# Performance work log

Measured on AMD Instinct MI355X. Metric: run time of the kernel, lower is better.

The kernel has to match this reference:

```python
import jax, jax.numpy as jnp
import numpy as np

C, NSET, K, GC = 64, 32, 3, 4
G = C // GC          # 16 KBA groups
EPS = 1e-6


def conv2d(x, w, b=None, groups=1, padding=0):
    out = jax.lax.conv_general_dilated(
        x, w, (1, 1), [(padding, padding), (padding, padding)],
        dimension_numbers=('NCHW', 'OIHW', 'NCHW'), feature_group_count=groups)
    if b is not None:
        out = out + b[None, :, None, None]
    return out


def layernorm2d(x, w, b):
    mu = jnp.mean(x, axis=1, keepdims=True)
    var = jnp.var(x, axis=1, keepdims=True)
    return (x - mu) / jnp.sqrt(var + EPS) * w[None, :, None, None] + b[None, :, None, None]


def simple_gate(x):
    a, b = jnp.split(x, 2, axis=1)
    return a * b


def kba(x, att, kb_b, kb_w):
    # x: [B,C,H,W], att: [B,nset,H,W], kb_b: [1,nset,C], kb_w: [1,nset,C*(C//G)*K*K]
    B, C_, H, W = x.shape
    KK = K * K
    cg = C_ // G  # channels per group
    att2 = att.reshape(B, NSET, H * W).transpose(0, 2, 1)            # [B,HW,nset]
    bias = att2 @ kb_b[0]                                             # [B,HW,C]
    attk = (att2 @ kb_w[0]).reshape(B, H * W, G, cg, cg * KK)         # per-pixel kernels
    pad = K // 2
    xp = jnp.pad(x, ((0, 0), (0, 0), (pad, pad), (pad, pad)))
    # torch.unfold ordering: feature index = c*KK + ki*K + kj
    patches = jnp.stack([xp[:, :, i:i + H, j:j + W]
                         for i in range(K) for j in range(K)], axis=2)  # [B,C,KK,H,W]
    uf = patches.reshape(B, G, cg * KK, H * W).transpose(0, 3, 1, 2)    # [B,HW,G,cg*KK]
    out = jnp.einsum('bpgod,bpgd->bpgo', attk, uf).reshape(B, H * W, C_) + bias
    return out.transpose(0, 2, 1).reshape(B, C_, H, W)


def fca(x, fc1_w, fc1_b, fc2_w, fc2_b, fsca_w, fsca_b):
    f = jnp.fft.fft2(x, norm='ortho')                      # over (H,W)
    cf = jnp.concatenate([f.real, f.imag], axis=1)         # [B,2C,H,W]
    t = conv2d(simple_gate(conv2d(cf, fc1_w, fc1_b)), fc2_w, fc2_b)
    r, im = jnp.split(t, 2, axis=1)
    ra = conv2d(jnp.mean(r, axis=(2, 3), keepdims=True), fsca_w, fsca_b)
    ia = conv2d(jnp.mean(im, axis=(2, 3), keepdims=True), fsca_w, fsca_b)
    fn = (r + r * ra) + 1j * (im + im * ia)
    return jnp.abs(jnp.fft.ifft2(fn, norm='ortho'))


def reference(inp, n1_w, n1_b, n2_w, n2_b, sca_w, sca_b, c11a_w, c11a_b, c11b_w, c11b_b,
              c1_w, c1_b, c21_w, c21_b, c2a_w, c2a_b, c2c_w, c2c_b, c211_w, c211_b,
              c3_w, c3_b, kb_w, kb_b, ga1, attgamma, beta, gamma,
              fc1_w, fc1_b, fc2_w, fc2_b, fsca_w, fsca_b):
    x = layernorm2d(inp, n1_w, n1_b)
    sca = conv2d(jnp.mean(x, axis=(2, 3), keepdims=True), sca_w, sca_b)
    x1 = conv2d(conv2d(x, c11a_w, c11a_b), c11b_w, c11b_b, groups=C // 4, padding=2)
    att = conv2d(simple_gate(conv2d(x, c2a_w, c2a_b, groups=32, padding=1)),
                 c2c_w, c2c_b) * attgamma + conv2d(x, c211_w, c211_b)
    uf = conv2d(conv2d(x, c1_w, c1_b), c21_w, c21_b, groups=C, padding=1)
    xk = kba(uf, att, kb_b, kb_w) * ga1 + uf
    x = xk * x1 * sca
    x = conv2d(x, c3_w, c3_b)
    y = inp + x * beta
    z = fca(layernorm2d(y, n2_w, n2_b), fc1_w, fc1_b, fc2_w, fc2_b, fsca_w, fsca_b)
    return y + z * gamma


def setup_inputs() -> dict:
    key = jax.random.key(0)
    B, H, W = 2, 160, 160
    ks = jax.random.split(key, 32)
    def rn(i, shape, s=0.05):
        return jax.random.normal(ks[i], shape, dtype=jnp.float32) * s
    return dict(
        inp=rn(0, (B, C, H, W), 1.0),
        n1_w=jnp.ones((C,), jnp.float32), n1_b=jnp.zeros((C,), jnp.float32),
        n2_w=jnp.ones((C,), jnp.float32), n2_b=jnp.zeros((C,), jnp.float32),
        sca_w=rn(1, (C, C, 1, 1)), sca_b=rn(2, (C,)),
        c11a_w=rn(3, (C, C, 1, 1)), c11a_b=rn(4, (C,)),
        c11b_w=rn(5, (C, 4, 5, 5)), c11b_b=rn(6, (C,)),
        c1_w=rn(7, (C, C, 1, 1)), c1_b=rn(8, (C,)),
        c21_w=rn(9, (C, 1, 3, 3)), c21_b=rn(10, (C,)),
        c2a_w=rn(11, (32, 2, 3, 3)), c2a_b=rn(12, (32,)),
        c2c_w=rn(13, (NSET, 16, 1, 1)), c2c_b=rn(14, (NSET,)),
        c211_w=rn(15, (NSET, C, 1, 1)), c211_b=rn(16, (NSET,)),
        c3_w=rn(17, (C, C, 1, 1)), c3_b=rn(18, (C,)),
        kb_w=rn(19, (1, NSET, C * (C // G) * K * K)),
        kb_b=rn(20, (1, NSET, C)),
        ga1=jnp.full((1, C, 1, 1), 0.01, jnp.float32),
        attgamma=jnp.full((1, NSET, 1, 1), 0.01, jnp.float32),
        beta=jnp.full((1, C, 1, 1), 0.01, jnp.float32),
        gamma=jnp.full((1, C, 1, 1), 0.01, jnp.float32),
        fc1_w=rn(21, (4 * C, 2 * C, 1, 1)), fc1_b=rn(22, (4 * C,)),
        fc2_w=rn(23, (2 * C, 2 * C, 1, 1)), fc2_b=rn(24, (2 * C,)),
        fsca_w=rn(25, (C, C, 1, 1)), fsca_b=rn(26, (C,)),
    )
```

## Files before the change

kernel.cpp:

```cpp
#include <hip/hip_runtime.h>
#include <hip/hip_bf16.h>

typedef __hip_bfloat16 bf16;
typedef __attribute__((ext_vector_type(8))) short short8;
typedef __attribute__((ext_vector_type(4))) float f32x4;
typedef __attribute__((ext_vector_type(4))) unsigned short u16x4;

#define Hh 160
#define Wd 160
#define HWp (Hh*Wd)
#define Bn 2
#define Cc 64
#define NPIX (Bn*HWp)
#define SCL 0.07905694150420949f
#define TWO_PI_160 0.039269908169872414f

static __device__ __forceinline__ float b2f(bf16 x) { return __bfloat162float(x); }
static __device__ __forceinline__ bf16 f2b(float f) { return __float2bfloat16(f); }
static __device__ __forceinline__ unsigned short f2bu(float f) {
  union { bf16 h; unsigned short u; } z; z.h = __float2bfloat16(f); return z.u;
}
static __device__ __forceinline__ float ubf(unsigned short u) {
  union { unsigned int i; float f; } z; z.i = ((unsigned int)u) << 16; return z.f;
}

__global__ void k_ln(const float* __restrict__ in, const float* __restrict__ w,
                     const float* __restrict__ bb, bf16* __restrict__ out) {
  __shared__ float2 sm[4][64];
  int t = threadIdx.x;
  int pxl = t & 63, cq = t >> 6;
  int pix = blockIdx.x * 64 + pxl;
  int b = pix / HWp, p = pix - b * HWp;
  const float* src = in + ((size_t)b * Cc + cq * 16) * HWp + p;
  float v[16];
  float s = 0.f, s2 = 0.f;
  #pragma unroll
  for (int i = 0; i < 16; i++) {
    v[i] = src[(size_t)i * HWp];
    s += v[i]; s2 += v[i] * v[i];
  }
  sm[cq][pxl] = make_float2(s, s2);
  __syncthreads();
  float S = 0.f, S2 = 0.f;
  #pragma unroll
  for (int k = 0; k < 4; k++) { float2 z = sm[k][pxl]; S += z.x; S2 += z.y; }
  float mu = S * (1.f / 64.f);
  float var = S2 * (1.f / 64.f) - mu * mu;
  float rs = rsqrtf(fmaxf(var, 0.f) + 1e-6f);
  bf16* dst = out + ((size_t)b * Cc + cq * 16) * HWp + p;
  #pragma unroll
  for (int i = 0; i < 16; i++) {
    int c = cq * 16 + i;
    dst[(size_t)i * HWp] = f2b((v[i] - mu) * rs * w[c] + bb[c]);
  }
}

__global__ void k_meanhw(const bf16* __restrict__ in, float* __restrict__ out) {
  int bc = blockIdx.x;
  const bf16* src = in + (size_t)bc * HWp;
  int t = threadIdx.x;
  float s = 0.f;
  for (int i = t; i < HWp; i += 256) s += b2f(src[i]);
  __shared__ float sm[256];
  sm[t] = s; __syncthreads();
  for (int off = 128; off; off >>= 1) { if (t < off) sm[t] += sm[t + off]; __syncthreads(); }
  if (t == 0) out[bc] = sm[0] * (1.f / HWp);
}

__global__ void k_meanhw2(const bf16* __restrict__ in0, const bf16* __restrict__ in1,
                          float* __restrict__ out) {
  int bc = blockIdx.x;
  const bf16* src = (bc < 128) ? (in0 + (size_t)bc * HWp) : (in1 + (size_t)(bc - 128) * HWp);
  int t = threadIdx.x;
  float s = 0.f;
  for (int i = t; i < HWp; i += 256) s += b2f(src[i]);
  __shared__ float sm[256];
  sm[t] = s; __syncthreads();
  for (int off = 128; off; off >>= 1) { if (t < off) sm[t] += sm[t + off]; __syncthreads(); }
  if (t == 0) out[bc] = sm[0] * (1.f / HWp);
}

__global__ void k_small_mv(const float* __restrict__ xin, const float* __restrict__ w,
                           const float* __restrict__ bias, float* __restrict__ out, int addone) {
  int t = threadIdx.x;
  int b = t >> 6, o = t & 63;
  float acc = bias[o];
  for (int k = 0; k < 64; k++) acc += w[o * 64 + k] * xin[b * 64 + k];
  out[t] = addone ? (1.f + acc) : acc;
}

__global__ void k_small_mv2(const float* __restrict__ xin, const float* __restrict__ w,
                            const float* __restrict__ bias, float* __restrict__ out) {
  int t = threadIdx.x;
  int half = t >> 7, r = t & 127;
  int b = r >> 6, o = r & 63;
  const float* x = xin + half * 128 + b * 64;
  float acc = bias[o];
  for (int k = 0; k < 64; k++) acc += w[o * 64 + k] * x[k];
  out[half * 128 + r] = 1.f + acc;
}

__global__ void k_c2a4(const bf16* __restrict__ in, const float* __restrict__ w,
                       const float* __restrict__ bias, bf16* __restrict__ out) {
  int t = threadIdx.x;
  int o = blockIdx.y, b = blockIdx.z;
  int pq = blockIdx.x * 256 + t;
  int h = pq / 40, x4 = (pq - h * 40) * 4;
  float bs = bias[o];
  float acc[4] = {bs, bs, bs, bs};
  #pragma unroll
  for (int ci = 0; ci < 2; ci++) {
    const unsigned short* src = (const unsigned short*)in + ((size_t)b * Cc + o * 2 + ci) * HWp;
    float wv[9];
    #pragma unroll
    for (int i = 0; i < 9; i++) wv[i] = w[(o * 2 + ci) * 9 + i];
    #pragma unroll
    for (int ki = 0; ki < 3; ki++) {
      int hh = h + ki - 1;
      if ((unsigned)hh >= Hh) continue;
      const unsigned short* row = src + hh * Wd + x4;
      float v[6];
      u16x4 m = *(const u16x4*)row;
      v[1] = ubf(m[0]); v[2] = ubf(m[1]); v[3] = ubf(m[2]); v[4] = ubf(m[3]);
      v[0] = (x4 > 0) ? ubf(row[-1]) : 0.f;
      v[5] = (x4 + 4 < Wd) ? ubf(row[4]) : 0.f;
      #pragma unroll
      for (int j = 0; j < 4; j++)
        #pragma unroll
        for (int kj = 0; kj < 3; kj++)
          acc[j] = fmaf(wv[ki * 3 + kj], v[j + kj], acc[j]);
    }
  }
  u16x4 pk;
  #pragma unroll
  for (int j = 0; j < 4; j++) pk[j] = f2bu(acc[j]);
  *(u16x4*)((unsigned short*)out + ((size_t)b * 32 + o) * HWp + h * Wd + x4) = pk;
}

__global__ void k_c21dw4(const bf16* __restrict__ in, const float* __restrict__ w,
                         const float* __restrict__ bias, bf16* __restrict__ out) {
  int t = threadIdx.x;
  int c = blockIdx.y, b = blockIdx.z;
  int pq = blockIdx.x * 256 + t;
  int h = pq / 40, x4 = (pq - h * 40) * 4;
  const unsigned short* src = (const unsigned short*)in + ((size_t)b * Cc + c) * HWp;
  float wv[9];
  #pragma unroll
  for (int i = 0; i < 9; i++) wv[i] = w[c * 9 + i];
  float bs = bias[c];
  float acc[4] = {bs, bs, bs, bs};
  #pragma unroll
  for (int ki = 0; ki < 3; ki++) {
    int hh = h + ki - 1;
    if ((unsigned)hh >= Hh) continue;
    const unsigned short* row = src + hh * Wd + x4;
    float v[6];
    u16x4 m = *(const u16x4*)row;
    v[1] = ubf(m[0]); v[2] = ubf(m[1]); v[3] = ubf(m[2]); v[4] = ubf(m[3]);
    v[0] = (x4 > 0) ? ubf(row[-1]) : 0.f;
    v[5] = (x4 + 4 < Wd) ? ubf(row[4]) : 0.f;
    #pragma unroll
    for (int j = 0; j < 4; j++)
      #pragma unroll
      for (int kj = 0; kj < 3; kj++)
        acc[j] = fmaf(wv[ki * 3 + kj], v[j + kj], acc[j]);
  }
  u16x4 pk;
  #pragma unroll
  for (int j = 0; j < 4; j++) pk[j] = f2bu(acc[j]);
  *(u16x4*)((unsigned short*)out + ((size_t)b * Cc + c) * HWp + h * Wd + x4) = pk;
}

__global__ void k_prep_all(const float* __restrict__ kbw, const float* __restrict__ kbb,
                           short* __restrict__ kbwF,
                           const float* __restrict__ fc1w, const float* __restrict__ fc2w,
                           short* __restrict__ wAf1, short* __restrict__ wAf2,
                           short* __restrict__ cosF, short* __restrict__ sinF,
                           const float* __restrict__ c11aw, const float* __restrict__ c1w,
                           const float* __restrict__ c3w, const float* __restrict__ c2cw,
                           const float* __restrict__ c211w, const float* __restrict__ attg,
                           short* __restrict__ wA_c11a, short* __restrict__ wA_c1,
                           short* __restrict__ wA_c3, short* __restrict__ wA_att) {
  int i = blockIdx.x * 256 + threadIdx.x;
  if (i < 81920) {
    int g = i / 5120, r = i - g * 5120;
    float v = 0.f;
    if (r < 4096) {
      int j = r & 7, lane = (r >> 3) & 63, mt = r >> 9;
      int m = mt * 16 + (lane & 15);
      int s = m >> 2, o = m & 3;
      int k = (lane >> 4) * 8 + j;
      v = kbw[s * 2304 + g * 144 + o * 36 + k];
    } else {
      int r2 = r - 4096;
      int j = r2 & 7, n = (r2 >> 3) & 15, mt = r2 >> 7;
      int m = mt * 16 + n;
      int s = m >> 2, o = m & 3;
      int k = 32 + j;
      if (k < 36) v = kbw[s * 2304 + g * 144 + o * 36 + k];
      else if (k == 36) v = kbb[s * 64 + g * 4 + o];
    }
    kbwF[i] = (short)f2bu(v);
  } else if (i < 131072) {
    int i1 = i - 81920;
    if (i1 < 32768) {
      int j = i1 & 7, lane = (i1 >> 3) & 63, fk = i1 >> 9;
      int kc = fk & 3, mt = fk >> 2;
      int o = mt * 16 + (lane & 15);
      int k = kc * 32 + (lane >> 4) * 8 + j;
      wAf1[i1] = (short)f2bu(fc1w[o * 128 + k]);
    } else {
      int i2 = i1 - 32768;
      int j = i2 & 7, lane = (i2 >> 3) & 63, fk = i2 >> 9;
      int kc = fk & 3, mt = fk >> 2;
      int o = mt * 16 + (lane & 15);
      int k = kc * 32 + (lane >> 4) * 8 + j;
      wAf2[i2] = (short)f2bu(fc2w[o * 128 + k]);
    }
  } else if (i < 156672) {
    int i2 = i - 131072;
    int j = i2 & 7, lane = (i2 >> 3) & 63, fk = i2 >> 9;
    int kc = fk % 5, ct = fk / 5;
    int c = ct * 16 + (lane & 15);
    int bb2 = kc * 32 + (lane >> 4) * 8 + j;
    int m = (bb2 * c) % 160;
    float sv, cv;
    __sincosf((float)m * TWO_PI_160, &sv, &cv);
    cosF[i2] = (short)f2bu(cv);
    sinF[i2] = (short)f2bu(sv);
  } else {
    int i3 = i - 156672;
    if (i3 < 12288) {
      int wi = i3 / 4096, r = i3 - wi * 4096;
      int j = r & 7, lane = (r >> 3) & 63, fk = r >> 9;
      int kc = fk & 1, mt = fk >> 1;
      int o = mt * 16 + (lane & 15);
      int k = kc * 32 + (lane >> 4) * 8 + j;
      const float* w = (wi == 0) ? c11aw : (wi == 1) ? c1w : c3w;
      short* dst = (wi == 0) ? wA_c11a : (wi == 1) ? wA_c1 : wA_c3;
      dst[r] = (short)f2bu(w[o * 64 + k]);
    } else {
      int r = i3 - 12288;
      int j = r & 7, lane = (r >> 3) & 63, fk = r >> 9;
      int kc = fk % 3, mt = fk / 3;
      int s = mt * 16 + (lane & 15);
      int k = kc * 32 + (lane >> 4) * 8 + j;
      float v;
      if (k < 16) v = c2cw[s * 16 + k] * attg[s];
      else if (k < 32) v = 0.f;
      else v = c211w[s * 64 + (k - 32)];
      wA_att[r] = (short)f2bu(v);
    }
  }
}

__global__ __launch_bounds__(256) void k_conv1x1_mfma(
    const bf16* __restrict__ in, const short* __restrict__ wA,
    const float* __restrict__ bias, bf16* __restrict__ out) {
  int b = blockIdx.z;
  int lane = threadIdx.x & 63, w = threadIdx.x >> 6;
  int px = blockIdx.x * 64 + w * 16 + (lane & 15);
  int q = lane >> 4;
  const unsigned short* src = (const unsigned short*)in + (size_t)b * Cc * HWp;
  const short8* wf = (const short8*)wA;
  f32x4 acc[4];
  #pragma unroll
  for (int mt = 0; mt < 4; mt++) acc[mt] = (f32x4){0.f, 0.f, 0.f, 0.f};
  #pragma unroll
  for (int kc = 0; kc < 2; kc++) {
    short8 bfv;
    #pragma unroll
    for (int j = 0; j < 8; j++) bfv[j] = (short)src[(size_t)(kc * 32 + q * 8 + j) * HWp + px];
    #pragma unroll
    for (int mt = 0; mt < 4; mt++) {
      short8 af = wf[(mt * 2 + kc) * 64 + lane];
      acc[mt] = __builtin_amdgcn_mfma_f32_16x16x32_bf16(af, bfv, acc[mt], 0, 0, 0);
    }
  }
  unsigned short* dst = (unsigned short*)out + (size_t)b * Cc * HWp;
  #pragma unroll
  for (int mt = 0; mt < 4; mt++)
    #pragma unroll
    for (int j = 0; j < 4; j++) {
      int o = mt * 16 + q * 4 + j;
      dst[(size_t)o * HWp + px] = f2bu(acc[mt][j] + bias[o]);
    }
}

__global__ __launch_bounds__(256) void k_c3y_mfma(
    const bf16* __restrict__ in, const short* __restrict__ wA,
    const float* __restrict__ bias, const float* __restrict__ beta,
    const float* __restrict__ inp, float* __restrict__ y) {
  int b = blockIdx.z;
  int lane = threadIdx.x & 63, w = threadIdx.x >> 6;
  int px = blockIdx.x * 64 + w * 16 + (lane & 15);
  int q = lane >> 4;
  const unsigned short* src = (const unsigned short*)in + (size_t)b * Cc * HWp;
  const short8* wf = (const short8*)wA;
  f32x4 acc[4];
  #pragma unroll
  for (int mt = 0; mt < 4; mt++) acc[mt] = (f32x4){0.f, 0.f, 0.f, 0.f};
  #pragma unroll
  for (int kc = 0; kc < 2; kc++) {
    short8 bfv;
    #pragma unroll
    for (int j = 0; j < 8; j++) bfv[j] = (short)src[(size_t)(kc * 32 + q * 8 + j) * HWp + px];
    #pragma unroll
    for (int mt = 0; mt < 4; mt++) {
      short8 af = wf[(mt * 2 + kc) * 64 + lane];
      acc[mt] = __builtin_amdgcn_mfma_f32_16x16x32_bf16(af, bfv, acc[mt], 0, 0, 0);
    }
  }
  #pragma unroll
  for (int mt = 0; mt < 4; mt++)
    #pragma unroll
    for (int j = 0; j < 4; j++) {
      int o = mt * 16 + q * 4 + j;
      size_t oi = ((size_t)b * Cc + o) * HWp + px;
      y[oi] = inp[oi] + (acc[mt][j] + bias[o]) * beta[o];
    }
}

__global__ __launch_bounds__(256) void k_att_mfma(
    const bf16* __restrict__ g, const bf16* __restrict__ x,
    const short* __restrict__ wA, const float* __restrict__ c2cb,
    const float* __restrict__ c211b, const float* __restrict__ attg,
    bf16* __restrict__ att) {
  int b = blockIdx.z;
  int lane = threadIdx.x & 63, w = threadIdx.x >> 6;
  int px = blockIdx.x * 64 + w * 16 + (lane & 15);
  int q = lane >> 4;
  const unsigned short* gs = (const unsigned short*)g + (size_t)b * 32 * HWp;
  const unsigned short* xs = (const unsigned short*)x + (size_t)b * Cc * HWp;
  const short8* wf = (const short8*)wA;
  f32x4 acc[2];
  acc[0] = (f32x4){0.f, 0.f, 0.f, 0.f};
  acc[1] = (f32x4){0.f, 0.f, 0.f, 0.f};
  {
    short8 bfv;
    #pragma unroll
    for (int j = 0; j < 8; j++) {
      int k = q * 8 + j;
      short v = 0;
      if (q < 2) {
        float gv = ubf(gs[(size_t)k * HWp + px]) * ubf(gs[(size_t)(16 + k) * HWp + px]);
        v = (short)f2bu(gv);
      }
      bfv[j] = v;
    }
    #pragma unroll
    for (int mt = 0; mt < 2; mt++) {
      short8 af = wf[(mt * 3 + 0) * 64 + lane];
      acc[mt] = __builtin_amdgcn_mfma_f32_16x16x32_bf16(af, bfv, acc[mt], 0, 0, 0);
    }
  }
  #pragma unroll
  for (int kc = 1; kc < 3; kc++) {
    short8 bfv;
    #pragma unroll
    for (int j = 0; j < 8; j++)
      bfv[j] = (short)xs[(size_t)((kc - 1) * 32 + q * 8 + j) * HWp + px];
    #pragma unroll
    for (int mt = 0; mt < 2; mt++) {
      short8 af = wf[(mt * 3 + kc) * 64 + lane];
      acc[mt] = __builtin_amdgcn_mfma_f32_16x16x32_bf16(af, bfv, acc[mt], 0, 0, 0);
    }
  }
  unsigned short* dst = (unsigned short*)att + (size_t)b * 32 * HWp;
  #pragma unroll
  for (int mt = 0; mt < 2; mt++)
    #pragma unroll
    for (int j = 0; j < 4; j++) {
      int s = mt * 16 + q * 4 + j;
      dst[(size_t)s * HWp + px] = f2bu(acc[mt][j] + c2cb[s] * attg[s] + c211b[s]);
    }
}

__global__ __launch_bounds__(256) void k_c11b_direct(
    const bf16* __restrict__ t1, const float* __restrict__ w,
    const float* __restrict__ bias, bf16* __restrict__ out) {
  __shared__ float xs[4 * 20 * 68];
  __shared__ float wsm[4 * 5 * 4 * 5];
  __shared__ float bsm[4];
  int bz = blockIdx.z;
  int b = bz >> 4, g = bz & 15;
  int h0 = blockIdx.y * 16;
  int w0 = blockIdx.x * 64;
  int t = threadIdx.x;
  for (int i = t; i < 400; i += 256) {
    int kj = i % 5, rem = i / 5;
    int o = rem & 3; rem >>= 2;
    int ki = rem % 5, ci = rem / 5;
    wsm[i] = w[((g * 4 + o) * 4 + ci) * 25 + ki * 5 + kj];
  }
  if (t < 4) bsm[t] = bias[g * 4 + t];
  const unsigned short* src = (const unsigned short*)t1 + ((size_t)b * Cc + g * 4) * HWp;
  for (int i = t; i < 4 * 20 * 68; i += 256) {
    int ci = i / 1360, rem2 = i - ci * 1360;
    int r = rem2 / 68, col = rem2 - r * 68;
    int hh = h0 + r - 2, ww = w0 + col - 2;
    float v = 0.f;
    if ((unsigned)hh < Hh && (unsigned)ww < Wd)
      v = ubf(src[(size_t)ci * HWp + hh * Wd + ww]);
    xs[i] = v;
  }
  __syncthreads();
  int wq = t & 15, hq = t >> 4;
  float acc[4][4];
  #pragma unroll
  for (int o = 0; o < 4; o++)
    #pragma unroll
    for (int j = 0; j < 4; j++) acc[o][j] = bsm[o];
  #pragma unroll
  for (int ci = 0; ci < 4; ci++) {
    #pragma unroll
    for (int ki = 0; ki < 5; ki++) {
      const float* wrow = &wsm[(ci * 5 + ki) * 20];
      float wv[20];
      #pragma unroll
      for (int x = 0; x < 20; x++) wv[x] = wrow[x];
      const float* xrow = &xs[ci * 1360 + (hq + ki) * 68 + wq * 4];
      float xv[8];
      #pragma unroll
      for (int x = 0; x < 8; x++) xv[x] = xrow[x];
      #pragma unroll
      for (int o = 0; o < 4; o++)
        #pragma unroll
        for (int j = 0; j < 4; j++)
          #pragma unroll
          for (int kj = 0; kj < 5; kj++)
            acc[o][j] = fmaf(wv[o * 5 + kj], xv[j + kj], acc[o][j]);
    }
  }
  int width = Wd - w0;
  if (wq * 4 < width) {
    unsigned short* dst = (unsigned short*)out + ((size_t)b * Cc + g * 4) * HWp
                        + (h0 + hq) * Wd + w0 + wq * 4;
    #pragma unroll
    for (int o = 0; o < 4; o++) {
      u16x4 pk;
      #pragma unroll
      for (int j = 0; j < 4; j++) pk[j] = f2bu(acc[o][j]);
      *(u16x4*)(dst + (size_t)o * HWp) = pk;
    }
  }
}

__global__ __launch_bounds__(256) void k_kba_mfma(
    const bf16* __restrict__ uf, const bf16* __restrict__ att,
    const bf16* __restrict__ x1, const float* __restrict__ scaV,
    const short* __restrict__ kbwF, const float* __restrict__ ga1,
    bf16* __restrict__ out) {
  __shared__ short8 fragL[1280];
  __shared__ unsigned short patchL[8 * 3 * 66];
  __shared__ unsigned short attL[64][33];
  int bz = blockIdx.z;
  int b = bz >> 3, gp = bz & 7;
  int h = blockIdx.y;
  int w0 = blockIdx.x * 64;
  int width = min(64, Wd - w0);
  int t = threadIdx.x;
  int c0 = gp * 8;
  const short8* src8 = (const short8*)kbwF + (size_t)gp * 1280;
  #pragma unroll
  for (int i = 0; i < 5; i++) fragL[t + i * 256] = src8[t + i * 256];
  const unsigned short* uf_u = (const unsigned short*)uf;
  for (int i = t; i < 8 * 3 * 66; i += 256) {
    int cl = i / 198, rem = i - cl * 198;
    int r = rem / 66, col = rem - r * 66;
    int hh = h + r - 1, ww = w0 + col - 1;
    unsigned short v = 0;
    if ((unsigned)hh < Hh && (unsigned)ww < Wd)
      v = uf_u[((size_t)b * Cc + c0 + cl) * HWp + hh * Wd + ww];
    patchL[i] = v;
  }
  const unsigned short* att_u = (const unsigned short*)att + (size_t)b * 32 * HWp;
  for (int i = t; i < 64 * 32; i += 256) {
    int px = i & 63, s = i >> 6;
    unsigned short v = 0;
    if (px < width) v = att_u[(size_t)s * HWp + h * Wd + w0 + px];
    attL[px][s] = v;
  }
  __syncthreads();
  int lane = t & 63, w = t >> 6;
  int n = lane & 15, q = lane >> 4;
  int pxl = w * 16 + n;
  float attR[8];
  #pragma unroll
  for (int mt = 0; mt < 8; mt++) attR[mt] = ubf(attL[pxl][4 * mt + q]);
  int offA[8];
  #pragma unroll
  for (int j = 0; j < 8; j++) {
    int k = q * 8 + j;
    int ci = k / 9, r = k - ci * 9, ki = r / 3, kj = r - ki * 3;
    offA[j] = ci * 198 + ki * 66 + pxl + kj;
  }
  int offB[4];
  #pragma unroll
  for (int j = 0; j < 4; j++) {
    int k = 32 + j, r = k - 27, ki = r / 3, kj = r - ki * 3;
    offB[j] = 3 * 198 + ki * 66 + pxl + kj;
  }
  const unsigned short* x1u = (const unsigned short*)x1 + (size_t)b * Cc * HWp + h * Wd + w0;
  unsigned short* outu = (unsigned short*)out + (size_t)b * Cc * HWp + h * Wd + w0;
  #pragma unroll
  for (int gl = 0; gl < 2; gl++) {
    int g = gp * 2 + gl;
    const short8* fgl = fragL + gl * 640;
    short8 b0, b1;
    #pragma unroll
    for (int j = 0; j < 8; j++) b0[j] = (short)patchL[gl * 792 + offA[j]];
    #pragma unroll
    for (int j = 0; j < 8; j++) b1[j] = 0;
    if (q == 0) {
      #pragma unroll
      for (int j = 0; j < 4; j++) b1[j] = (short)patchL[gl * 792 + offB[j]];
      b1[4] = (short)0x3F80;
    }
    f32x4 acc[8];
    #pragma unroll
    for (int mt = 0; mt < 8; mt++) acc[mt] = (f32x4){0.f, 0.f, 0.f, 0.f};
    #pragma unroll
    for (int mt = 0; mt < 8; mt++) {
      short8 a0 = fgl[mt * 64 + lane];
      acc[mt] = __builtin_amdgcn_mfma_f32_16x16x32_bf16(a0, b0, acc[mt], 0, 0, 0);
      short8 a1 = (short8){0,0,0,0,0,0,0,0};
      if (q == 0) a1 = fgl[512 + mt * 16 + n];
      acc[mt] = __builtin_amdgcn_mfma_f32_16x16x32_bf16(a1, b1, acc[mt], 0, 0, 0);
    }
    #pragma unroll
    for (int o = 0; o < 4; o++) {
      float P = 0.f;
      #pragma unroll
      for (int mt = 0; mt < 8; mt++) P += attR[mt] * acc[mt][o];
      P += __shfl_xor(P, 16);
      P += __shfl_xor(P, 32);
      if (o == q && pxl < width) {
        int c = g * 4 + q;
        float ufc = ubf(patchL[(gl * 4 + q) * 198 + 66 + pxl + 1]);
        float xk = P * ga1[c] + ufc;
        float xv = xk * ubf(x1u[(size_t)c * HWp + pxl]) * scaV[b * 64 + c];
        outu[(size_t)c * HWp + pxl] = f2bu(xv);
      }
    }
  }
}

__global__ void k_ln2(const float* __restrict__ in, const float* __restrict__ w,
                      const float* __restrict__ bb, bf16* __restrict__ out) {
  __shared__ float2 sm[4][64];
  int t = threadIdx.x;
  int pxl = t & 63, cq = t >> 6;
  int pix = blockIdx.x * 64 + pxl;
  int b = pix / HWp, p = pix - b * HWp;
  const float* src = in + ((size_t)b * Cc + cq * 16) * HWp + p;
  float v[16];
  float s = 0.f, s2 = 0.f;
  #pragma unroll
  for (int i = 0; i < 16; i++) {
    v[i] = src[(size_t)i * HWp];
    s += v[i]; s2 += v[i] * v[i];
  }
  sm[cq][pxl] = make_float2(s, s2);
  __syncthreads();
  float S = 0.f, S2 = 0.f;
  #pragma unroll
  for (int k = 0; k < 4; k++) { float2 z = sm[k][pxl]; S += z.x; S2 += z.y; }
  float mu = S * (1.f / 64.f);
  float var = S2 * (1.f / 64.f) - mu * mu;
  float rs = rsqrtf(fmaxf(var, 0.f) + 1e-6f);
  bf16* dst = out + ((size_t)b * Cc + cq * 16) * HWp + p;
  #pragma unroll
  for (int i = 0; i < 16; i++) {
    int c = cq * 16 + i;
    dst[(size_t)i * HWp] = f2b((v[i] - mu) * rs * w[c] + bb[c]);
  }
}

__global__ __launch_bounds__(64) void k_cpass_mfma(
    const bf16* __restrict__ inr, const bf16* __restrict__ ini,
    const short* __restrict__ cosF, const short* __restrict__ sinF,
    bf16* __restrict__ outr, bf16* __restrict__ outi,
    float sgn, float scale,
    const float* __restrict__ sclr, const float* __restrict__ scli) {
  int plane = blockIdx.z;
  int a0 = blockIdx.x * 16;
  int cth = blockIdx.y * 5;
  int lane = threadIdx.x;
  int n = lane & 15, q = lane >> 4;
  const unsigned short* pr = (const unsigned short*)inr + (size_t)plane * HWp;
  const unsigned short* pi = ini ? (const unsigned short*)ini + (size_t)plane * HWp : nullptr;
  float srm = sclr ? sclr[plane] : 1.f;
  float sim = scli ? scli[plane] : 1.f;
  short8 br[5], bi[5];
  #pragma unroll
  for (int kc = 0; kc < 5; kc++) {
    br[kc] = *(const short8*)(pr + (a0 + n) * 160 + kc * 32 + q * 8);
    if (pi) bi[kc] = *(const short8*)(pi + (a0 + n) * 160 + kc * 32 + q * 8);
  }
  const short8* cf = (const short8*)cosF;
  const short8* sf = (const short8*)sinF;
  unsigned short* qr = (unsigned short*)outr + (size_t)plane * HWp;
  unsigned short* qi = (unsigned short*)outi + (size_t)plane * HWp;
  for (int ctl = 0; ctl < 5; ctl++) {
    int ct = cth + ctl;
    f32x4 arr = (f32x4){0.f,0.f,0.f,0.f}, asr = (f32x4){0.f,0.f,0.f,0.f};
    f32x4 ari = (f32x4){0.f,0.f,0.f,0.f}, asi = (f32x4){0.f,0.f,0.f,0.f};
    #pragma unroll
    for (int kc = 0; kc < 5; kc++) {
      short8 ca = cf[(ct * 5 + kc) * 64 + lane];
      short8 sa = sf[(ct * 5 + kc) * 64 + lane];
      arr = __builtin_amdgcn_mfma_f32_16x16x32_bf16(ca, br[kc], arr, 0, 0, 0);
      asr = __builtin_amdgcn_mfma_f32_16x16x32_bf16(sa, br[kc], asr, 0, 0, 0);
      if (pi) {
        ari = __builtin_amdgcn_mfma_f32_16x16x32_bf16(ca, bi[kc], ari, 0, 0, 0);
        asi = __builtin_amdgcn_mfma_f32_16x16x32_bf16(sa, bi[kc], asi, 0, 0, 0);
      }
    }
    #pragma unroll
    for (int j = 0; j < 4; j++) {
      int c = ct * 16 + q * 4 + j;
      float xc = srm * arr[j], xs = srm * asr[j];
      float ic = pi ? sim * ari[j] : 0.f, is = pi ? sim * asi[j] : 0.f;
      float orv = (xc - sgn * is) * scale;
      float oiv = (sgn * xs + ic) * scale;
      qr[c * 160 + a0 + n] = f2bu(orv);
      qi[c * 160 + a0 + n] = f2bu(oiv);
    }
  }
}

__global__ __launch_bounds__(64) void k_cpass_final_mfma(
    const bf16* __restrict__ inr, const bf16* __restrict__ ini,
    const short* __restrict__ cosF, const short* __restrict__ sinF,
    float sgn, float scale,
    const float* __restrict__ gamma, float* __restrict__ dout) {
  int plane = blockIdx.z;
  int a0 = blockIdx.x * 16;
  int cth = blockIdx.y * 5;
  int lane = threadIdx.x;
  int n = lane & 15, q = lane >> 4;
  const unsigned short* pr = (const unsigned short*)inr + (size_t)plane * HWp;
  const unsigned short* pi = (const unsigned short*)ini + (size_t)plane * HWp;
  short8 br[5], bi[5];
  #pragma unroll
  for (int kc = 0; kc < 5; kc++) {
    br[kc] = *(const short8*)(pr + (a0 + n) * 160 + kc * 32 + q * 8);
    bi[kc] = *(const short8*)(pi + (a0 + n) * 160 + kc * 32 + q * 8);
  }
  const short8* cf = (const short8*)cosF;
  const short8* sf = (const short8*)sinF;
  float gm = gamma[plane & 63];
  float* dp = dout + (size_t)plane * HWp;
  for (int ctl = 0; ctl < 5; ctl++) {
    int ct = cth + ctl;
    f32x4 arr = (f32x4){0.f,0.f,0.f,0.f}, asr = (f32x4){0.f,0.f,0.f,0.f};
    f32x4 ari = (f32x4){0.f,0.f,0.f,0.f}, asi = (f32x4){0.f,0.f,0.f,0.f};
    #pragma unroll
    for (int kc = 0; kc < 5; kc++) {
      short8 ca = cf[(ct * 5 + kc) * 64 + lane];
      short8 sa = sf[(ct * 5 + kc) * 64 + lane];
      arr = __builtin_amdgcn_mfma_f32_16x16x32_bf16(ca, br[kc], arr, 0, 0, 0);
      asr = __builtin_amdgcn_mfma_f32_16x16x32_bf16(sa, br[kc], asr, 0, 0, 0);
      ari = __builtin_amdgcn_mfma_f32_16x16x32_bf16(ca, bi[kc], ari, 0, 0, 0);
      asi = __builtin_amdgcn_mfma_f32_16x16x32_bf16(sa, bi[kc], asi, 0, 0, 0);
    }
    #pragma unroll
    for (int j = 0; j < 4; j++) {
      int c = ct * 16 + q * 4 + j;
      float orv = (arr[j] - sgn * asi[j]) * scale;
      float oiv = (sgn * asr[j] + ari[j]) * scale;
      float z = sqrtf(orv * orv + oiv * oiv);
      dp[c * 160 + a0 + n] += z * gm;
    }
  }
}

__global__ __launch_bounds__(256) void k_fc1_mfma(
    const bf16* __restrict__ Fr, const bf16* __restrict__ Fi,
    const short* __restrict__ wA, const float* __restrict__ bias,
    bf16* __restrict__ G1, bf16* __restrict__ G2) {
  int b = blockIdx.z;
  int lane = threadIdx.x & 63, w = threadIdx.x >> 6;
  int px = blockIdx.x * 64 + w * 16 + (lane & 15);
  int q = lane >> 4;
  const unsigned short* fr = (const unsigned short*)Fr + (size_t)b * Cc * HWp;
  const unsigned short* fi = (const unsigned short*)Fi + (size_t)b * Cc * HWp;
  const short8* wf = (const short8*)wA;
  f32x4 acc[16];
  #pragma unroll
  for (int mt = 0; mt < 16; mt++) acc[mt] = (f32x4){0.f, 0.f, 0.f, 0.f};
  #pragma unroll
  for (int kc = 0; kc < 4; kc++) {
    const unsigned short* basep = (kc < 2) ? (fr + (size_t)(kc * 32) * HWp)
                                           : (fi + (size_t)((kc - 2) * 32) * HWp);
    short8 bfv;
    #pragma unroll
    for (int j = 0; j < 8; j++) bfv[j] = (short)basep[(size_t)(q * 8 + j) * HWp + px];
    #pragma unroll
    for (int mt = 0; mt < 16; mt++) {
      short8 af = wf[(mt * 4 + kc) * 64 + lane];
      acc[mt] = __builtin_amdgcn_mfma_f32_16x16x32_bf16(af, bfv, acc[mt], 0, 0, 0);
    }
  }
  unsigned short* g1 = (unsigned short*)G1 + (size_t)b * Cc * HWp;
  unsigned short* g2 = (unsigned short*)G2 + (size_t)b * Cc * HWp;
  #pragma unroll
  for (int mt = 0; mt < 8; mt++)
    #pragma unroll
    for (int j = 0; j < 4; j++) {
      int o = mt * 16 + q * 4 + j;
      float v1 = acc[mt][j] + bias[o];
      float v2 = acc[mt + 8][j] + bias[o + 128];
      unsigned short hv = f2bu(v1 * v2);
      if (o < 64) g1[(size_t)o * HWp + px] = hv;
      else        g2[(size_t)(o - 64) * HWp + px] = hv;
    }
}

__global__ __launch_bounds__(256) void k_fc2_mfma(
    const bf16* __restrict__ G1, const bf16* __restrict__ G2,
    const short* __restrict__ wA, const float* __restrict__ bias,
    bf16* __restrict__ Or, bf16* __restrict__ Oi) {
  int b = blockIdx.z;
  int lane = threadIdx.x & 63, w = threadIdx.x >> 6;
  int px = blockIdx.x * 64 + w * 16 + (lane & 15);
  int q = lane >> 4;
  const unsigned short* g1 = (const unsigned short*)G1 + (size_t)b * Cc * HWp;
  const unsigned short* g2 = (const unsigned short*)G2 + (size_t)b * Cc * HWp;
  const short8* wf = (const short8*)wA;
  f32x4 acc[8];
  #pragma unroll
  for (int mt = 0; mt < 8; mt++) acc[mt] = (f32x4){0.f, 0.f, 0.f, 0.f};
  #pragma unroll
  for (int kc = 0; kc < 4; kc++) {
    const unsigned short* basep = (kc < 2) ? (g1 + (size_t)(kc * 32) * HWp)
                                           : (g2 + (size_t)((kc - 2) * 32) * HWp);
    short8 bfv;
    #pragma unroll
    for (int j = 0; j < 8; j++) bfv[j] = (short)basep[(size_t)(q * 8 + j) * HWp + px];
    #pragma unroll
    for (int mt = 0; mt < 8; mt++) {
      short8 af = wf[(mt * 4 + kc) * 64 + lane];
      acc[mt] = __builtin_amdgcn_mfma_f32_16x16x32_bf16(af, bfv, acc[mt], 0, 0, 0);
    }
  }
  unsigned short* orp = (unsigned short*)Or + (size_t)b * Cc * HWp;
  unsigned short* oip = (unsigned short*)Oi + (size_t)b * Cc * HWp;
  #pragma unroll
  for (int mt = 0; mt < 8; mt++)
    #pragma unroll
    for (int j = 0; j < 4; j++) {
      int o = mt * 16 + q * 4 + j;
      unsigned short hv = f2bu(acc[mt][j] + bias[o]);
      if (o < 64) orp[(size_t)o * HWp + px] = hv;
      else        oip[(size_t)(o - 64) * HWp + px] = hv;
    }
}

extern "C" void kernel_launch(void* const* d_in, const int* in_sizes, int n_in,
                              void* d_out, int out_size, void* d_ws, size_t ws_size,
                              hipStream_t stream) {
  const float* inp   = (const float*)d_in[0];
  const float* n1w   = (const float*)d_in[1];
  const float* n1b   = (const float*)d_in[2];
  const float* n2w   = (const float*)d_in[3];
  const float* n2b   = (const float*)d_in[4];
  const float* scaw  = (const float*)d_in[5];
  const float* scab  = (const float*)d_in[6];
  const float* c11aw = (const float*)d_in[7];
  const float* c11ab = (const float*)d_in[8];
  const float* c11bw = (const float*)d_in[9];
  const float* c11bb = (const float*)d_in[10];
  const float* c1w   = (const float*)d_in[11];
  const float* c1b   = (const float*)d_in[12];
  const float* c21w  = (const float*)d_in[13];
  const float* c21b  = (const float*)d_in[14];
  const float* c2aw  = (const float*)d_in[15];
  const float* c2ab  = (const float*)d_in[16];
  const float* c2cw  = (const float*)d_in[17];
  const float* c2cb  = (const float*)d_in[18];
  const float* c211w = (const float*)d_in[19];
  const float* c211b = (const float*)d_in[20];
  const float* c3w   = (const float*)d_in[21];
  const float* c3b   = (const float*)d_in[22];
  const float* kbw   = (const float*)d_in[23];
  const float* kbb   = (const float*)d_in[24];
  const float* ga1   = (const float*)d_in[25];
  const float* attg  = (const float*)d_in[26];
  const float* beta  = (const float*)d_in[27];
  const float* gamma = (const float*)d_in[28];
  const float* fc1w  = (const float*)d_in[29];
  const float* fc1b  = (const float*)d_in[30];
  const float* fc2w  = (const float*)d_in[31];
  const float* fc2b  = (const float*)d_in[32];
  const float* fscaw = (const float*)d_in[33];
  const float* fscab = (const float*)d_in[34];

  const size_t S = (size_t)Bn * Cc * HWp;
  bf16* A  = (bf16*)d_ws;
  bf16* Bs = A + S;
  bf16* Cs = A + 2 * S;
  bf16* Ds = A + 3 * S;
  float* smalls = (float*)(A + 4 * S);
  float* xm   = smalls;
  float* scaV = smalls + 128;
  float* rmv  = smalls + 256;
  float* sra  = smalls + 512;
  short* wS   = (short*)(smalls + 1024);
  short* wAf1 = wS;
  short* wAf2 = wAf1 + 32768;
  short* cosF = wAf2 + 16384;
  short* sinF = cosF + 25600;
  short* wA_c11a = sinF + 25600;
  short* wA_c1   = wA_c11a + 4096;
  short* wA_c3   = wA_c1 + 4096;
  short* wA_att  = wA_c3 + 4096;
  short* kbwF    = wA_att + 3072;
  bf16* gbuf = Bs;
  bf16* attb = Bs + S / 2;
  float* yb  = (float*)d_out;

  dim3 cgrid(10, 2, Bn * Cc);
  dim3 pgrid(400, 1, Bn);

  k_prep_all<<<dim3(672), dim3(256), 0, stream>>>(kbw, kbb, kbwF, fc1w, fc2w, wAf1, wAf2,
                                                  cosF, sinF, c11aw, c1w, c3w, c2cw, c211w,
                                                  attg, wA_c11a, wA_c1, wA_c3, wA_att);
  k_ln<<<dim3(800), dim3(256), 0, stream>>>(inp, n1w, n1b, A);
  k_meanhw<<<dim3(128), dim3(256), 0, stream>>>(A, xm);
  k_small_mv<<<dim3(1), dim3(128), 0, stream>>>(xm, scaw, scab, scaV, 0);
  k_conv1x1_mfma<<<pgrid, dim3(256), 0, stream>>>(A, wA_c11a, c11ab, Bs);
  k_c11b_direct<<<dim3(3, 10, Bn * 16), dim3(256), 0, stream>>>(Bs, c11bw, c11bb, Cs);
  k_c2a4<<<dim3(25, 32, Bn), dim3(256), 0, stream>>>(A, c2aw, c2ab, gbuf);
  k_att_mfma<<<pgrid, dim3(256), 0, stream>>>(gbuf, A, wA_att, c2cb, c211b, attg, attb);
  k_conv1x1_mfma<<<pgrid, dim3(256), 0, stream>>>(A, wA_c1, c1b, Ds);
  k_c21dw4<<<dim3(25, 64, Bn), dim3(256), 0, stream>>>(Ds, c21w, c21b, A);
  k_kba_mfma<<<dim3(3, 160, Bn * 8), dim3(256), 0, stream>>>(A, attb, Cs, scaV, kbwF, ga1, Ds);
  k_c3y_mfma<<<pgrid, dim3(256), 0, stream>>>(Ds, wA_c3, c3b, beta, inp, yb);
  k_ln2<<<dim3(800), dim3(256), 0, stream>>>(yb, n2w, n2b, A);
  k_cpass_mfma<<<cgrid, dim3(64), 0, stream>>>(A, (const bf16*)nullptr, cosF, sinF, Bs, Cs, -1.f, SCL, nullptr, nullptr);
  k_cpass_mfma<<<cgrid, dim3(64), 0, stream>>>(Bs, Cs, cosF, sinF, Ds, A, -1.f, SCL, nullptr, nullptr);
  k_fc1_mfma<<<pgrid, dim3(256), 0, stream>>>(Ds, A, wAf1, fc1b, Bs, Cs);
  k_fc2_mfma<<<pgrid, dim3(256), 0, stream>>>(Bs, Cs, wAf2, fc2b, Ds, A);
  k_meanhw2<<<dim3(256), dim3(256), 0, stream>>>(Ds, A, rmv);
  k_small_mv2<<<dim3(1), dim3(256), 0, stream>>>(rmv, fscaw, fscab, sra);
  k_cpass_mfma<<<cgrid, dim3(64), 0, stream>>>(Ds, A, cosF, sinF, Bs, Cs, 1.f, SCL, sra, sra + 128);
  k_cpass_final_mfma<<<cgrid, dim3(64), 0, stream>>>(Bs, Cs, cosF, sinF, 1.f, SCL, gamma, yb);
}
```

Measured before the change: 445.1 us.

## Fuse spatial-mean reductions and second layernorm into producer kernels

Drops the separate mean-over-HW kernels by accumulating per-channel means with wavefront shuffles and atomics inside the first layernorm and the fc2 kernel, with the accumulators zeroed in the prep kernel. Also fuses the second layernorm into the c3 residual kernel, reducing over the 64 output channels held across lanes of each wave. This removes three launches and re-reads of full activation tensors. The cost is many global and shared atomics, plus float summation order that is no longer deterministic.

```diff
diff --git a/kernel.cpp b/kernel.cpp
--- a/kernel.cpp
+++ b/kernel.cpp
@@ -25,7 +25,8 @@
 }
 
 __global__ void k_ln(const float* __restrict__ in, const float* __restrict__ w,
-                     const float* __restrict__ bb, bf16* __restrict__ out) {
+                     const float* __restrict__ bb, bf16* __restrict__ out,
+                     float* __restrict__ xm) {
   __shared__ float2 sm[4][64];
   int t = threadIdx.x;
   int pxl = t & 63, cq = t >> 6;
@@ -51,33 +52,13 @@
   #pragma unroll
   for (int i = 0; i < 16; i++) {
     int c = cq * 16 + i;
-    dst[(size_t)i * HWp] = f2b((v[i] - mu) * rs * w[c] + bb[c]);
-  }
-}
-
-__global__ void k_meanhw(const bf16* __restrict__ in, float* __restrict__ out) {
-  int bc = blockIdx.x;
-  const bf16* src = in + (size_t)bc * HWp;
-  int t = threadIdx.x;
-  float s = 0.f;
-  for (int i = t; i < HWp; i += 256) s += b2f(src[i]);
-  __shared__ float sm[256];
-  sm[t] = s; __syncthreads();
-  for (int off = 128; off; off >>= 1) { if (t < off) sm[t] += sm[t + off]; __syncthreads(); }
-  if (t == 0) out[bc] = sm[0] * (1.f / HWp);
-}
-
-__global__ void k_meanhw2(const bf16* __restrict__ in0, const bf16* __restrict__ in1,
-                          float* __restrict__ out) {
-  int bc = blockIdx.x;
-  const bf16* src = (bc < 128) ? (in0 + (size_t)bc * HWp) : (in1 + (size_t)(bc - 128) * HWp);
-  int t = threadIdx.x;
-  float s = 0.f;
-  for (int i = t; i < HWp; i += 256) s += b2f(src[i]);
-  __shared__ float sm[256];
-  sm[t] = s; __syncthreads();
-  for (int off = 128; off; off >>= 1) { if (t < off) sm[t] += sm[t + off]; __syncthreads(); }
-  if (t == 0) out[bc] = sm[0] * (1.f / HWp);
+    float val = (v[i] - mu) * rs * w[c] + bb[c];
+    dst[(size_t)i * HWp] = f2b(val);
+    float r = val;
+    r += __shfl_xor(r, 1);  r += __shfl_xor(r, 2);  r += __shfl_xor(r, 4);
+    r += __shfl_xor(r, 8);  r += __shfl_xor(r, 16); r += __shfl_xor(r, 32);
+    if (pxl == 0) atomicAdd(&xm[b * 64 + c], r * (1.f / HWp));
+  }
 }
 
 __global__ void k_small_mv(const float* __restrict__ xin, const float* __restrict__ w,
@@ -180,7 +161,10 @@
                            const float* __restrict__ c3w, const float* __restrict__ c2cw,
                            const float* __restrict__ c211w, const float* __restrict__ attg,
                            short* __restrict__ wA_c11a, short* __restrict__ wA_c1,
-                           short* __restrict__ wA_c3, short* __restrict__ wA_att) {
+                           short* __restrict__ wA_c3, short* __restrict__ wA_att,
+                           float* __restrict__ xm, float* __restrict__ rmv) {
+  if (blockIdx.x == 0 && threadIdx.x < 128) xm[threadIdx.x] = 0.f;
+  if (blockIdx.x == 1) rmv[threadIdx.x] = 0.f;
   int i = blockIdx.x * 256 + threadIdx.x;
   if (i < 81920) {
     int g = i / 5120, r = i - g * 5120;
@@ -287,10 +271,12 @@
     }
 }
 
-__global__ __launch_bounds__(256) void k_c3y_mfma(
+__global__ __launch_bounds__(256) void k_c3y_ln2(
     const bf16* __restrict__ in, const short* __restrict__ wA,
     const float* __restrict__ bias, const float* __restrict__ beta,
-    const float* __restrict__ inp, float* __restrict__ y) {
+    const float* __restrict__ inp, float* __restrict__ y,
+    const float* __restrict__ n2w, const float* __restrict__ n2b,
+    bf16* __restrict__ Xout) {
   int b = blockIdx.z;
   int lane = threadIdx.x & 63, w = threadIdx.x >> 6;
   int px = blockIdx.x * 64 + w * 16 + (lane & 15);
@@ -311,13 +297,31 @@
       acc[mt] = __builtin_amdgcn_mfma_f32_16x16x32_bf16(af, bfv, acc[mt], 0, 0, 0);
     }
   }
+  float yv[4][4];
+  float s = 0.f, s2 = 0.f;
   #pragma unroll
   for (int mt = 0; mt < 4; mt++)
     #pragma unroll
     for (int j = 0; j < 4; j++) {
       int o = mt * 16 + q * 4 + j;
       size_t oi = ((size_t)b * Cc + o) * HWp + px;
-      y[oi] = inp[oi] + (acc[mt][j] + bias[o]) * beta[o];
+      float v = inp[oi] + (acc[mt][j] + bias[o]) * beta[o];
+      y[oi] = v;
+      yv[mt][j] = v;
+      s += v; s2 += v * v;
+    }
+  s  += __shfl_xor(s, 16);  s  += __shfl_xor(s, 32);
+  s2 += __shfl_xor(s2, 16); s2 += __shfl_xor(s2, 32);
+  float mu = s * (1.f / 64.f);
+  float var = s2 * (1.f / 64.f) - mu * mu;
+  float rs = rsqrtf(fmaxf(var, 0.f) + 1e-6f);
+  unsigned short* Xu = (unsigned short*)Xout + (size_t)b * Cc * HWp;
+  #pragma unroll
+  for (int mt = 0; mt < 4; mt++)
+    #pragma unroll
+    for (int j = 0; j < 4; j++) {
+      int o = mt * 16 + q * 4 + j;
+      Xu[(size_t)o * HWp + px] = f2bu((yv[mt][j] - mu) * rs * n2w[o] + n2b[o]);
     }
 }
 
@@ -546,37 +550,6 @@
   }
 }
 
-__global__ void k_ln2(const float* __restrict__ in, const float* __restrict__ w,
-                      const float* __restrict__ bb, bf16* __restrict__ out) {
-  __shared__ float2 sm[4][64];
-  int t = threadIdx.x;
-  int pxl = t & 63, cq = t >> 6;
-  int pix = blockIdx.x * 64 + pxl;
-  int b = pix / HWp, p = pix - b * HWp;
-  const float* src = in + ((size_t)b * Cc + cq * 16) * HWp + p;
-  float v[16];
-  float s = 0.f, s2 = 0.f;
-  #pragma unroll
-  for (int i = 0; i < 16; i++) {
-    v[i] = src[(size_t)i * HWp];
-    s += v[i]; s2 += v[i] * v[i];
-  }
-  sm[cq][pxl] = make_float2(s, s2);
-  __syncthreads();
-  float S = 0.f, S2 = 0.f;
-  #pragma unroll
-  for (int k = 0; k < 4; k++) { float2 z = sm[k][pxl]; S += z.x; S2 += z.y; }
-  float mu = S * (1.f / 64.f);
-  float var = S2 * (1.f / 64.f) - mu * mu;
-  float rs = rsqrtf(fmaxf(var, 0.f) + 1e-6f);
-  bf16* dst = out + ((size_t)b * Cc + cq * 16) * HWp + p;
-  #pragma unroll
-  for (int i = 0; i < 16; i++) {
-    int c = cq * 16 + i;
-    dst[(size_t)i * HWp] = f2b((v[i] - mu) * rs * w[c] + bb[c]);
-  }
-}
-
 __global__ __launch_bounds__(64) void k_cpass_mfma(
     const bf16* __restrict__ inr, const bf16* __restrict__ ini,
     const short* __restrict__ cosF, const short* __restrict__ sinF,
@@ -721,11 +694,15 @@
 __global__ __launch_bounds__(256) void k_fc2_mfma(
     const bf16* __restrict__ G1, const bf16* __restrict__ G2,
     const short* __restrict__ wA, const float* __restrict__ bias,
-    bf16* __restrict__ Or, bf16* __restrict__ Oi) {
+    bf16* __restrict__ Or, bf16* __restrict__ Oi, float* __restrict__ rmv) {
+  __shared__ float psum[128];
   int b = blockIdx.z;
-  int lane = threadIdx.x & 63, w = threadIdx.x >> 6;
+  int t = threadIdx.x;
+  int lane = t & 63, w = t >> 6;
   int px = blockIdx.x * 64 + w * 16 + (lane & 15);
   int q = lane >> 4;
+  if (t < 128) psum[t] = 0.f;
+  __syncthreads();
   const unsigned short* g1 = (const unsigned short*)G1 + (size_t)b * Cc * HWp;
   const unsigned short* g2 = (const unsigned short*)G2 + (size_t)b * Cc * HWp;
   const short8* wf = (const short8*)wA;
@@ -747,15 +724,27 @@
   }
   unsigned short* orp = (unsigned short*)Or + (size_t)b * Cc * HWp;
   unsigned short* oip = (unsigned short*)Oi + (size_t)b * Cc * HWp;
+  int n = lane & 15;
   #pragma unroll
   for (int mt = 0; mt < 8; mt++)
     #pragma unroll
     for (int j = 0; j < 4; j++) {
       int o = mt * 16 + q * 4 + j;
-      unsigned short hv = f2bu(acc[mt][j] + bias[o]);
+      float v = acc[mt][j] + bias[o];
+      unsigned short hv = f2bu(v);
       if (o < 64) orp[(size_t)o * HWp + px] = hv;
       else        oip[(size_t)(o - 64) * HWp + px] = hv;
-    }
+      float r = v;
+      r += __shfl_xor(r, 1); r += __shfl_xor(r, 2);
+      r += __shfl_xor(r, 4); r += __shfl_xor(r, 8);
+      if (n == 0) atomicAdd(&psum[o], r);
+    }
+  __syncthreads();
+  if (t < 128) {
+    int o = t;
+    int idx = (o < 64) ? (b * 64 + o) : (128 + b * 64 + (o - 64));
+    atomicAdd(&rmv[idx], psum[o] * (1.f / HWp));
+  }
 }
 
 extern "C" void kernel_launch(void* const* d_in, const int* in_sizes, int n_in,
@@ -826,9 +815,8 @@
 
   k_prep_all<<<dim3(672), dim3(256), 0, stream>>>(kbw, kbb, kbwF, fc1w, fc2w, wAf1, wAf2,
                                                   cosF, sinF, c11aw, c1w, c3w, c2cw, c211w,
-                                                  attg, wA_c11a, wA_c1, wA_c3, wA_att);
-  k_ln<<<dim3(800), dim3(256), 0, stream>>>(inp, n1w, n1b, A);
-  k_meanhw<<<dim3(128), dim3(256), 0, stream>>>(A, xm);
+                                                  attg, wA_c11a, wA_c1, wA_c3, wA_att, xm, rmv);
+  k_ln<<<dim3(800), dim3(256), 0, stream>>>(inp, n1w, n1b, A, xm);
   k_small_mv<<<dim3(1), dim3(128), 0, stream>>>(xm, scaw, scab, scaV, 0);
   k_conv1x1_mfma<<<pgrid, dim3(256), 0, stream>>>(A, wA_c11a, c11ab, Bs);
   k_c11b_direct<<<dim3(3, 10, Bn * 16), dim3(256), 0, stream>>>(Bs, c11bw, c11bb, Cs);
@@ -837,13 +825,11 @@
   k_conv1x1_mfma<<<pgrid, dim3(256), 0, stream>>>(A, wA_c1, c1b, Ds);
   k_c21dw4<<<dim3(25, 64, Bn), dim3(256), 0, stream>>>(Ds, c21w, c21b, A);
   k_kba_mfma<<<dim3(3, 160, Bn * 8), dim3(256), 0, stream>>>(A, attb, Cs, scaV, kbwF, ga1, Ds);
-  k_c3y_mfma<<<pgrid, dim3(256), 0, stream>>>(Ds, wA_c3, c3b, beta, inp, yb);
-  k_ln2<<<dim3(800), dim3(256), 0, stream>>>(yb, n2w, n2b, A);
+  k_c3y_ln2<<<pgrid, dim3(256), 0, stream>>>(Ds, wA_c3, c3b, beta, inp, yb, n2w, n2b, A);
   k_cpass_mfma<<<cgrid, dim3(64), 0, stream>>>(A, (const bf16*)nullptr, cosF, sinF, Bs, Cs, -1.f, SCL, nullptr, nullptr);
   k_cpass_mfma<<<cgrid, dim3(64), 0, stream>>>(Bs, Cs, cosF, sinF, Ds, A, -1.f, SCL, nullptr, nullptr);
   k_fc1_mfma<<<pgrid, dim3(256), 0, stream>>>(Ds, A, wAf1, fc1b, Bs, Cs);
-  k_fc2_mfma<<<pgrid, dim3(256), 0, stream>>>(Bs, Cs, wAf2, fc2b, Ds, A);
-  k_meanhw2<<<dim3(256), dim3(256), 0, stream>>>(Ds, A, rmv);
+  k_fc2_mfma<<<pgrid, dim3(256), 0, stream>>>(Bs, Cs, wAf2, fc2b, Ds, A, rmv);
   k_small_mv2<<<dim3(1), dim3(256), 0, stream>>>(rmv, fscaw, fscab, sra);
   k_cpass_mfma<<<cgrid, dim3(64), 0, stream>>>(Ds, A, cosF, sinF, Bs, Cs, 1.f, SCL, sra, sra + 128);
   k_cpass_final_mfma<<<cgrid, dim3(64), 0, stream>>>(Bs, Cs, cosF, sinF, 1.f, SCL, gamma, yb);
```

After: 561.5 us. 1.26x slower.
